# Kernel optimization log

Hardware: AMD Instinct MI355X
Metric: run time of the kernel (lower is better)

Reference implementation:

```python
import jax, jax.numpy as jnp
import numpy as np

BETA = 10.0
DTAU = 0.01
LTAU = int(round(BETA / DTAU))  # 1000
N_NODES = 256
N_IWN = 256
BATCH = 16
N_POLES = 16
ZETA3 = 1.2020569031595942  # zeta(3)
ZETA5 = 1.0369277551433699  # zeta(5)

# Constant buffers (match torch register_buffer contents)
_taus = np.linspace(0.0, BETA - DTAU, LTAU).astype(np.float32)
_nodes, _w = np.polynomial.legendre.leggauss(N_NODES)
_phi = np.tan(np.pi / 2.0 * _nodes).astype(np.float32)
_weights = _w.astype(np.float32)
_iwn = (1j * (2 * np.arange(N_IWN) + 1) * np.pi / BETA).astype(np.complex64)
_coefs = np.array([
    -0.5,
    -BETA / 4.0,
    -7.0 * ZETA3 * BETA**2 / (4.0 * np.pi**3),
    BETA**3 / 48.0,
    31.0 * ZETA5 * BETA**4 / (16.0 * np.pi**5),
], dtype=np.float32)


def setup_inputs() -> dict:
    key = jax.random.key(0)
    k1, k2, k3, k4 = jax.random.split(key, 4)
    poles_re = jax.random.normal(k1, (BATCH, N_POLES), jnp.float32)
    # gamma = -Im(poles) must be > 0 for physical (damped) poles
    poles_im = -(jax.random.uniform(k2, (BATCH, N_POLES), jnp.float32) + 0.1)
    residues_re = 0.5 * jax.random.normal(k3, (BATCH, N_POLES), jnp.float32)
    residues_im = 0.5 * jax.random.normal(k4, (BATCH, N_POLES), jnp.float32)
    return {"poles_re": poles_re, "poles_im": poles_im,
            "residues_re": residues_re, "residues_im": residues_im}


def reference(poles_re, poles_im, residues_re, residues_im):
    taus = jnp.asarray(_taus)          # [L]
    phi = jnp.asarray(_phi)            # [N]
    weights = jnp.asarray(_weights)    # [N]
    iwn = jnp.asarray(_iwn)            # [Nw] complex64
    coefs = jnp.asarray(_coefs)        # [5]

    eps = poles_re                     # Re(poles)  [B,P]
    gam = -poles_im                    # -Im(poles) [B,P]
    a = residues_re
    b = residues_im

    # Gauss-Legendre quadrature over substituted frequency axis
    omegas = eps[..., None] + gam[..., None] * phi            # [B,P,N]
    numer = 0.5 * (a[..., None] - b[..., None] * phi)         # [B,P,N]
    arg1 = jnp.clip(taus[None, None, :, None] * omegas[:, :, None, :], -50.0, 50.0)
    arg2 = jnp.clip((taus - BETA)[None, None, :, None] * omegas[:, :, None, :], -50.0, 50.0)
    denom = jnp.exp(arg1) + jnp.exp(arg2)                     # [B,P,L,N]
    integrand = (numer[:, :, None, :] / denom).sum(axis=1)    # [B,L,N]
    G_tau = integrand @ weights                               # [B,L] real

    # Matsubara series with asymptotic tail corrections for G_tau[:,0]
    z = eps - 1j * gam                                        # [B,P] complex64
    res = a + 1j * b
    G_iwn = (res[:, :, None] / (z[:, :, None] - iwn[None, None, :])).sum(axis=1)  # [B,Nw]

    c = -res
    G_iwn = G_iwn - (jnp.real(c)[:, :, None] / iwn[None, None, :]).sum(axis=1)
    G0 = coefs[0] * jnp.real(c).sum(axis=1)
    c = c * z
    G_iwn = G_iwn - (c[:, :, None] / iwn[None, None, :] ** 2).sum(axis=1)
    G0 = G0 + coefs[1] * jnp.real(c).sum(axis=1)
    c = c * z
    G_iwn = G_iwn - (c[:, :, None] / iwn[None, None, :] ** 3).sum(axis=1)
    G0 = G0 + coefs[2] * jnp.imag(c).sum(axis=1)
    c = c * z
    G_iwn = G_iwn - (c[:, :, None] / iwn[None, None, :] ** 4).sum(axis=1)
    G0 = G0 + coefs[3] * jnp.real(c).sum(axis=1)
    c = c * z
    G_iwn = G_iwn - (c[:, :, None] / iwn[None, None, :] ** 5).sum(axis=1)
    G0 = G0 + coefs[4] * jnp.imag(c).sum(axis=1)

    G0 = G0 + 2.0 * jnp.real(G_iwn.sum(axis=1)) / BETA
    return G_tau.at[:, 0].set(G0)
```

## Files before the change

kernel.cpp:

```cpp
#include <hip/hip_runtime.h>
#include <math.h>

#define BETA   10.0f
#define LTAU   1000
#define NNODES 256
#define BATCH  16
#define NPOLES 16
#define TCHUNK 25
#define NBLK_T (LTAU / TCHUNK)

#if __has_builtin(__builtin_amdgcn_exp2f)
#define EXP2F(x) __builtin_amdgcn_exp2f(x)
#else
#define EXP2F(x) exp2f(x)
#endif

#if __has_builtin(__builtin_amdgcn_rcpf)
#define RCPF(x) __builtin_amdgcn_rcpf(x)
#else
#define RCPF(x) (1.0f / (x))
#endif

struct GLTable { float phi[NNODES]; float wts[NNODES]; };

static GLTable compute_gl_table() {
    GLTable T;
    const int n = NNODES;
    for (int k = 0; k < n / 2; ++k) {
        double x = cos(M_PI * ((double)k + 0.75) / ((double)n + 0.5));
        double p1 = x, p0 = 1.0, dpn = 1.0;
        for (int it = 0; it < 5; ++it) {
            p0 = 1.0; p1 = x;
            for (int m = 1; m < n; ++m) {
                const double p2 = ((2.0 * m + 1.0) * x * p1 - (double)m * p0)
                                  / ((double)m + 1.0);
                p0 = p1; p1 = p2;
            }
            dpn = n * (x * p1 - p0) / (x * x - 1.0);
            x  -= p1 / dpn;
        }
        const double w  = 2.0 / ((1.0 - x * x) * dpn * dpn);
        const double ph = tan(0.5 * M_PI * x);
        const int hi = n - 1 - k;
        T.phi[hi] = (float)ph;   T.wts[hi] = (float)w;
        T.phi[k]  = (float)(-ph); T.wts[k]  = (float)w;
    }
    return T;
}

static const GLTable g_gl_table = compute_gl_table();

__global__ __launch_bounds__(256) void fused_kernel(const GLTable T,
                                                    const float* __restrict__ pr,
                                                    const float* __restrict__ pim,
                                                    const float* __restrict__ rr,
                                                    const float* __restrict__ ri,
                                                    float* __restrict__ out) {
    const int b   = blockIdx.y;
    const int tid = threadIdx.x;

    if (blockIdx.x < NBLK_T) {
        const int l0 = blockIdx.x * TCHUNK;
        const float LOG2E = 1.4426950408889634f;

        const float ph  = T.phi[tid];
        const float wn2 = 0.5f * T.wts[tid];

        float o2[NPOLES], qq[NPOLES], nmS[NPOLES];
        #pragma unroll
        for (int p = 0; p < NPOLES; ++p) {
            const float eps = pr[b * NPOLES + p];
            const float gam = -pim[b * NPOLES + p];
            const float av  = rr[b * NPOLES + p];
            const float bv  = ri[b * NPOLES + p];
            const float o   = fmaf(gam, ph, eps) * LOG2E;
            const float bo  = 10.0f * o;
            o2[p] = o;
            qq[p] = fminf(bo, 0.0f);
            const float S = RCPF(1.0f + EXP2F(-fabsf(bo)));
            nmS[p] = fmaf(-bv, ph, av) * S;
        }

        __shared__ float partial[TCHUNK][4];
        const int lane = tid & 63;
        const int wid  = tid >> 6;

        #pragma unroll 2
        for (int j = 0; j < TCHUNK; ++j) {
            const float ntau = -0.01f * (float)(l0 + j);
            float s0 = 0.0f, s1 = 0.0f;
            #pragma unroll
            for (int p = 0; p < NPOLES; p += 2) {
                const float x0 = fmaf(ntau, o2[p],     qq[p]);
                const float x1 = fmaf(ntau, o2[p + 1], qq[p + 1]);
                s0 = fmaf(nmS[p],     EXP2F(x0), s0);
                s1 = fmaf(nmS[p + 1], EXP2F(x1), s1);
            }
            float v = wn2 * (s0 + s1);
            #pragma unroll
            for (int o = 32; o > 0; o >>= 1) v += __shfl_down(v, o, 64);
            if (lane == 0) partial[j][wid] = v;
        }
        __syncthreads();

        if (tid < TCHUNK && (l0 + tid) > 0) {
            out[b * LTAU + l0 + tid] =
                partial[tid][0] + partial[tid][1] + partial[tid][2] + partial[tid][3];
        }
    } else {
        const int t = tid;

        double S1r = 0.0, C2r = 0.0, C3i = 0.0, C4r = 0.0, C5i = 0.0;
        for (int p = 0; p < NPOLES; ++p) {
            const double eps = (double)pr[b * NPOLES + p];
            const double gam = -(double)pim[b * NPOLES + p];
            const double a   = (double)rr[b * NPOLES + p];
            const double bb  = (double)ri[b * NPOLES + p];
            const double zr = eps, zi = -gam;
            double cr = -a, ci = -bb;
            S1r += cr;
            double nr = cr * zr - ci * zi, ni = cr * zi + ci * zr;
            cr = nr; ci = ni;  C2r += cr;
            nr = cr * zr - ci * zi; ni = cr * zi + ci * zr;
            cr = nr; ci = ni;  C3i += ci;
            nr = cr * zr - ci * zi; ni = cr * zi + ci * zr;
            cr = nr; ci = ni;  C4r += cr;
            nr = cr * zr - ci * zi; ni = cr * zi + ci * zr;
            cr = nr; ci = ni;  C5i += ci;
        }

        const double y = (2.0 * t + 1.0) * M_PI / (double)BETA;
        double re = 0.0;
        for (int p = 0; p < NPOLES; ++p) {
            const double eps = (double)pr[b * NPOLES + p];
            const double gy  = -(double)pim[b * NPOLES + p] + y;
            const double a   = (double)rr[b * NPOLES + p];
            const double bb  = (double)ri[b * NPOLES + p];
            re += (a * eps - bb * gy) / (eps * eps + gy * gy);
        }
        const double y2 = y * y;
        re += C2r / y2 + C3i / (y2 * y) - C4r / (y2 * y2) - C5i / (y2 * y2 * y);

        double v = re;
        #pragma unroll
        for (int o = 32; o > 0; o >>= 1) v += __shfl_down(v, o, 64);
        __shared__ double smd[4];
        const int lane = t & 63, wid = t >> 6;
        if (lane == 0) smd[wid] = v;
        __syncthreads();

        if (t == 0) {
            const double tot = smd[0] + smd[1] + smd[2] + smd[3];
            const double ZETA3 = 1.2020569031595942;
            const double ZETA5 = 1.0369277551433699;
            const double B = (double)BETA;
            const double c0 = -0.5;
            const double c1 = -B / 4.0;
            const double c2 = -7.0 * ZETA3 * B * B / (4.0 * M_PI * M_PI * M_PI);
            const double c3 = B * B * B / 48.0;
            const double c4 = 31.0 * ZETA5 * B * B * B * B /
                              (16.0 * M_PI * M_PI * M_PI * M_PI * M_PI);
            const double G0 = c0 * S1r + c1 * C2r + c2 * C3i + c3 * C4r + c4 * C5i
                            + 2.0 * tot / B;
            out[b * LTAU] = (float)G0;
        }
    }
}

extern "C" void kernel_launch(void* const* d_in, const int* in_sizes, int n_in,
                              void* d_out, int out_size, void* d_ws, size_t ws_size,
                              hipStream_t stream) {
    const float* poles_re    = (const float*)d_in[0];
    const float* poles_im    = (const float*)d_in[1];
    const float* residues_re = (const float*)d_in[2];
    const float* residues_im = (const float*)d_in[3];
    float* out = (float*)d_out;

    dim3 grid(NBLK_T + 1, BATCH);
    fused_kernel<<<grid, 256, 0, stream>>>(g_gl_table, poles_re, poles_im,
                                           residues_re, residues_im, out);
}
```

Baseline: 73.26 us.

## Replace per-tau exp with geometric recurrence, DPP wave reduction, smaller tau chunks

Each block now computes the exponential once at its first tau and steps it forward by a per-pole multiplicative ratio, so the inner loop does multiply-adds with no transcendental calls. The wave reduction uses DPP row operations in place of shuffle-down, and the weight is folded into the numerator. TCHUNK drops to 10, giving more blocks with shorter recurrence chains, and launch bounds request 6 blocks per CU. Repeated multiplication adds rounding drift, and the clamped ratio differs from the reference's per-tau clipping of the exponent.

```diff
diff --git a/kernel.cpp b/kernel.cpp
--- a/kernel.cpp
+++ b/kernel.cpp
@@ -6,7 +6,7 @@
 #define NNODES 256
 #define BATCH  16
 #define NPOLES 16
-#define TCHUNK 25
+#define TCHUNK 10
 #define NBLK_T (LTAU / TCHUNK)
 
 #if __has_builtin(__builtin_amdgcn_exp2f)
@@ -50,23 +50,41 @@
 
 static const GLTable g_gl_table = compute_gl_table();
 
-__global__ __launch_bounds__(256) void fused_kernel(const GLTable T,
-                                                    const float* __restrict__ pr,
-                                                    const float* __restrict__ pim,
-                                                    const float* __restrict__ rr,
-                                                    const float* __restrict__ ri,
-                                                    float* __restrict__ out) {
+__device__ __forceinline__ float wave64_sum_dpp(float v) {
+    int t;
+    t = __builtin_amdgcn_update_dpp(0, __float_as_int(v), 0x111, 0xf, 0xf, true);
+    v += __int_as_float(t);
+    t = __builtin_amdgcn_update_dpp(0, __float_as_int(v), 0x112, 0xf, 0xf, true);
+    v += __int_as_float(t);
+    t = __builtin_amdgcn_update_dpp(0, __float_as_int(v), 0x114, 0xf, 0xf, true);
+    v += __int_as_float(t);
+    t = __builtin_amdgcn_update_dpp(0, __float_as_int(v), 0x118, 0xf, 0xf, true);
+    v += __int_as_float(t);
+    t = __builtin_amdgcn_update_dpp(0, __float_as_int(v), 0x142, 0xa, 0xf, true);
+    v += __int_as_float(t);
+    t = __builtin_amdgcn_update_dpp(0, __float_as_int(v), 0x143, 0xc, 0xf, true);
+    v += __int_as_float(t);
+    return v;
+}
+
+__global__ __launch_bounds__(256, 6) void fused_kernel(const GLTable T,
+                                                       const float* __restrict__ pr,
+                                                       const float* __restrict__ pim,
+                                                       const float* __restrict__ rr,
+                                                       const float* __restrict__ ri,
+                                                       float* __restrict__ out) {
     const int b   = blockIdx.y;
     const int tid = threadIdx.x;
 
     if (blockIdx.x < NBLK_T) {
         const int l0 = blockIdx.x * TCHUNK;
         const float LOG2E = 1.4426950408889634f;
+        const float ntau0 = -0.01f * (float)l0;
 
         const float ph  = T.phi[tid];
         const float wn2 = 0.5f * T.wts[tid];
 
-        float o2[NPOLES], qq[NPOLES], nmS[NPOLES];
+        float E[NPOLES], d[NPOLES], nmS[NPOLES];
         #pragma unroll
         for (int p = 0; p < NPOLES; ++p) {
             const float eps = pr[b * NPOLES + p];
@@ -75,10 +93,12 @@
             const float bv  = ri[b * NPOLES + p];
             const float o   = fmaf(gam, ph, eps) * LOG2E;
             const float bo  = 10.0f * o;
-            o2[p] = o;
-            qq[p] = fminf(bo, 0.0f);
-            const float S = RCPF(1.0f + EXP2F(-fabsf(bo)));
-            nmS[p] = fmaf(-bv, ph, av) * S;
+            const float q   = fminf(bo, 0.0f);
+            const float S   = RCPF(1.0f + EXP2F(-fabsf(bo)));
+            nmS[p] = fmaf(-bv, ph, av) * S * wn2;
+            const float dx = fminf(fmaxf(-0.01f * o, -125.0f), 125.0f);
+            d[p] = EXP2F(dx);
+            E[p] = EXP2F(fmaf(ntau0, o, q));
         }
 
         __shared__ float partial[TCHUNK][4];
@@ -87,19 +107,14 @@
 
         #pragma unroll 2
         for (int j = 0; j < TCHUNK; ++j) {
-            const float ntau = -0.01f * (float)(l0 + j);
             float s0 = 0.0f, s1 = 0.0f;
             #pragma unroll
             for (int p = 0; p < NPOLES; p += 2) {
-                const float x0 = fmaf(ntau, o2[p],     qq[p]);
-                const float x1 = fmaf(ntau, o2[p + 1], qq[p + 1]);
-                s0 = fmaf(nmS[p],     EXP2F(x0), s0);
-                s1 = fmaf(nmS[p + 1], EXP2F(x1), s1);
+                s0 = fmaf(nmS[p],     E[p],     s0);  E[p]     *= d[p];
+                s1 = fmaf(nmS[p + 1], E[p + 1], s1);  E[p + 1] *= d[p + 1];
             }
-            float v = wn2 * (s0 + s1);
-            #pragma unroll
-            for (int o = 32; o > 0; o >>= 1) v += __shfl_down(v, o, 64);
-            if (lane == 0) partial[j][wid] = v;
+            const float v = wave64_sum_dpp(s0 + s1);
+            if (lane == 63) partial[j][wid] = v;
         }
         __syncthreads();
 
```

New measurement: 67.27 us. 8.2% less time.
